# Kernel optimization log

Measured on AMD Instinct MI355X. Metric: run time of the kernel, lower is better.

## Reference

```python
import jax, jax.numpy as jnp
import numpy as np

B, C, H, W = 16, 256, 64, 64
E = 8           # num_experts
TOPK = 2
HID = int(C * 2.0)  # hidden_mult = 2.0 -> 512


def setup_inputs() -> dict:
    key = jax.random.key(0)
    ks = jax.random.split(key, 6)
    x = jax.random.normal(ks[0], (B, C, H, W), dtype=jnp.float32)
    Wr = jax.random.normal(ks[1], (C, E), dtype=jnp.float32) * 0.02
    br = jnp.zeros((E,), dtype=jnp.float32)
    W1 = jax.random.normal(ks[2], (E, C, HID), dtype=jnp.float32) * 0.02
    b1 = jnp.zeros((E, HID), dtype=jnp.float32)
    W2 = jax.random.normal(ks[3], (E, HID, C), dtype=jnp.float32) * 0.02
    b2 = jnp.zeros((E, C), dtype=jnp.float32)
    # nn.Parameter(torch.zeros(1)) in the original; use a small random value so
    scale = jax.random.normal(ks[4], (1,), dtype=jnp.float32) * 0.1
    return {"x": x, "Wr": Wr, "br": br, "W1": W1, "b1": b1,
            "W2": W2, "b2": b2, "scale": scale}


def reference(x, Wr, br, W1, b1, W2, b2, scale):
    b, c, h, w = x.shape
    tokens = jnp.transpose(x, (0, 2, 3, 1)).reshape(b, h * w, c)  # (B, T, C)
    logits = tokens @ Wr + br                                      # (B, T, E)
    topv, topi = jax.lax.top_k(logits, TOPK)                       # (B, T, K)
    wts = jax.nn.softmax(topv, axis=-1)                            # (B, T, K)

    out = jnp.zeros_like(tokens)
    num_experts = Wr.shape[1]
    for e in range(num_experts):
        # combine weight for expert e: sum of routing weights where selected
        we = jnp.sum(jnp.where(topi == e, wts, 0.0), axis=-1)      # (B, T)
        hdn = jax.nn.gelu(tokens @ W1[e] + b1[e], approximate=False)
        y = hdn @ W2[e] + b2[e]                                    # (B, T, C)
        out = out + y * we[..., None]

    out = jnp.transpose(out.reshape(b, h, w, c), (0, 3, 1, 2))     # (B, C, H, W)
    return x + scale[0] * out
```

## Files before the change

### kernel.cpp

```cpp
#include <hip/hip_runtime.h>
#include <hip/hip_bf16.h>
#include <math.h>

#define HW   4096
#define CCH  256
#define NE   8
#define HID  512
#define NTOK 65536
#define PADH 260

typedef short s16x8 __attribute__((ext_vector_type(8)));
typedef float f32x4 __attribute__((ext_vector_type(4)));
typedef unsigned short u16x8 __attribute__((ext_vector_type(8)));

__device__ __forceinline__ float fast_gelu(float v) {
    float v2 = v * v;
    float s  = v * fmaf(0.10294324f, v2, 2.3022079f);
    float e  = exp2f(-s);
    return v * __builtin_amdgcn_rcpf(1.0f + e);
}

__device__ __forceinline__ float bfbits2f(unsigned short h) {
    return __uint_as_float(((unsigned)h) << 16);
}

__global__ __launch_bounds__(256) void k_transpose_both(
    const float* __restrict__ W1, const float* __restrict__ W2,
    __hip_bfloat16* __restrict__ w1t, __hip_bfloat16* __restrict__ w2t,
    int* __restrict__ meta)
{
    __shared__ float t[64][65];
    if (blockIdx.x == 0 && threadIdx.x < 16) meta[threadIdx.x] = 0;
    int bb = blockIdx.x;
    const float* in; __hip_bfloat16* out; int R, CC;
    if (bb < 256) { in = W1; out = w1t; R = 256; CC = 512; }
    else          { in = W2; out = w2t; R = 512; CC = 256; bb -= 256; }
    int tilesC = CC >> 6;
    int per = (R >> 6) * tilesC;
    int e = bb / per, tt = bb % per;
    int r0 = (tt / tilesC) << 6, c0 = (tt % tilesC) << 6;
    const float* ip = in + (size_t)e * R * CC;
    __hip_bfloat16* op = out + (size_t)e * R * CC;
    int lane = threadIdx.x & 63, g = threadIdx.x >> 6;
    for (int i = 0; i < 16; i++) {
        int r = i * 4 + g;
        t[r][lane] = ip[(size_t)(r0 + r) * CC + c0 + lane];
    }
    __syncthreads();
    for (int i = 0; i < 16; i++) {
        int r = i * 4 + g;
        op[(size_t)(c0 + r) * R + r0 + lane] = __float2bfloat16(t[lane][r]);
    }
}

__global__ __launch_bounds__(256) void k_router(
    const float* __restrict__ x, const float* __restrict__ Wr, const float* __restrict__ br,
    __hip_bfloat16* __restrict__ tokens, int* __restrict__ pair, float2* __restrict__ wts,
    int* __restrict__ meta )
{
    __shared__ float xt[CCH][66];
    __shared__ float wr[CCH][NE];
    __shared__ float lg[64][NE];
    __shared__ int lc[NE];
    int tid = threadIdx.x;
    int n0 = blockIdx.x * 64;
    int b = n0 >> 12, p0 = n0 & 4095;
    const float* xb = x + (size_t)b * CCH * HW + p0;
    for (int i = tid; i < CCH * NE; i += 256) ((float*)wr)[i] = Wr[i];
    if (tid < NE) lc[tid] = 0;
    int lane = tid & 63, wv = tid >> 6;
    {
        int j2 = tid & 31, cg = tid >> 5;
        for (int i = 0; i < 32; i++) {
            int c = cg + 8 * i;
            float2 v = *(const float2*)(xb + (size_t)c * HW + 2 * j2);
            *(float2*)&xt[c][2 * j2] = v;
        }
    }
    __syncthreads();
    float a0 = br[2 * wv], a1 = br[2 * wv + 1];
    for (int c = 0; c < CCH; c++) {
        float xv = xt[c][lane];
        a0 = fmaf(xv, wr[c][2 * wv], a0);
        a1 = fmaf(xv, wr[c][2 * wv + 1], a1);
    }
    lg[lane][2 * wv] = a0;
    lg[lane][2 * wv + 1] = a1;
    __syncthreads();
    if (wv == 0) {
        float v0 = -1e30f, v1 = -1e30f; int i0 = 0, i1 = 0;
        for (int e = 0; e < NE; e++) {
            float l = lg[lane][e];
            if (l > v0)      { v1 = v0; i1 = i0; v0 = l; i0 = e; }
            else if (l > v1) { v1 = l; i1 = e; }
        }
        float e1 = expf(v1 - v0);
        float s = 1.0f + e1;
        wts[n0 + lane] = make_float2(1.0f / s, e1 / s);
        pair[n0 + lane] = i0 | (i1 << 8);
        atomicAdd(&lc[i0], 1);
        atomicAdd(&lc[i1], 1);
    }
    __syncthreads();
    if (tid < NE && lc[tid] > 0) atomicAdd(&meta[tid], lc[tid]);
    for (int r = 0; r < 64; r++)
        tokens[(size_t)(n0 + r) * CCH + tid] = __float2bfloat16(xt[tid][r]);
}

__global__ __launch_bounds__(256) void k_scatter(
    const int* __restrict__ pair, const float2* __restrict__ wts,
    int* __restrict__ meta, int* __restrict__ assign_tok, float* __restrict__ assign_w,
    int2* __restrict__ tok_slots)
{
    __shared__ int lcount[NE];
    __shared__ int lbase[NE];
    __shared__ int soff[NE];
    int tid = threadIdx.x;
    int n = blockIdx.x * 256 + tid;
    if (tid < NE) lcount[tid] = 0;
    __syncthreads();
    int pr = pair[n];
    int e0 = pr & 0xff, e1 = (pr >> 8) & 0xff;
    int p0 = atomicAdd(&lcount[e0], 1);
    int p1 = atomicAdd(&lcount[e1], 1);
    __syncthreads();
    if (tid == 0) {
        int off = 0, toff = 0;
        for (int ee = 0; ee < NE; ee++) {
            soff[ee] = off;
            int c = meta[ee];
            if (blockIdx.x == 0) { meta[16 + ee] = off; meta[25 + ee] = toff; }
            off += c;
            toff += (c + 63) >> 6;
        }
        if (blockIdx.x == 0) { meta[24] = off; meta[33] = toff; meta[34] = toff; }
    }
    if (tid < NE) lbase[tid] = atomicAdd(&meta[8 + tid], lcount[tid]);
    __syncthreads();
    float2 w = wts[n];
    int s0 = soff[e0] + lbase[e0] + p0;
    int s1 = soff[e1] + lbase[e1] + p1;
    assign_tok[s0] = n; assign_w[s0] = w.x;
    assign_tok[s1] = n; assign_w[s1] = w.y;
    tok_slots[n] = make_int2(s0, s1);
}

__global__ __launch_bounds__(512, 4) void k_expert(
    const __hip_bfloat16* __restrict__ tokens,
    const __hip_bfloat16* __restrict__ w1t,
    const __hip_bfloat16* __restrict__ w2t,
    const float* __restrict__ b1, const float* __restrict__ b2,
    const int* __restrict__ meta,
    const int* __restrict__ assign_tok, const float* __restrict__ assign_w,
    __hip_bfloat16* __restrict__ ybuf)
{
    __shared__ __align__(16) __hip_bfloat16 Af[64 * 256];
    __shared__ __align__(16) __hip_bfloat16 Hs[64 * PADH];
    __shared__ float wrow[64];
    __shared__ int trow[64];

    int total = meta[34];
    int bid = (blockIdx.x & 7) * 257 + (blockIdx.x >> 3);
    if (bid >= total) return;
    int e = 0;
    while (e < 7 && bid >= meta[25 + e + 1]) e++;
    int tile = bid - meta[25 + e];
    int cnt = meta[e];
    int r0 = tile << 6;
    int abase = meta[16 + e] + r0;
    int nrows = cnt - r0; if (nrows > 64) nrows = 64;

    int tid = threadIdx.x;
    if (tid < 64) {
        if (tid < nrows) { trow[tid] = assign_tok[abase + tid]; wrow[tid] = assign_w[abase + tid]; }
        else             { trow[tid] = 0; wrow[tid] = 0.0f; }
    }
    __syncthreads();

    {
        uint4* dst = (uint4*)Af;
#pragma unroll
        for (int j = 0; j < 4; j++) {
            int row = j * 16 + (tid & 15);
            int chunk = (tid >> 4) & 31;
            dst[j * 512 + tid] = ((const uint4*)(tokens + (size_t)trow[row] * CCH))[chunk];
        }
    }

    int lane = tid & 63, wv = tid >> 6;
    int quad = lane >> 4, l15 = lane & 15;

    const __hip_bfloat16* w1e = w1t + (size_t)e * HID * CCH;
    const __hip_bfloat16* w2e = w2t + (size_t)e * CCH * HID;
    const float* b1e = b1 + e * HID;
    const float* b2e = b2 + e * CCH;

    const s16x8* apb = (const s16x8*)Af + quad * 16 + l15;

    const s16x8* bq0h[2]; const s16x8* bq1h[2];
#pragma unroll
    for (int h = 0; h < 2; h++) {
        int c0 = h * 256 + wv * 32;
        bq0h[h] = (const s16x8*)(w1e + (size_t)(c0)      * CCH + (size_t)l15 * CCH + quad * 8);
        bq1h[h] = (const s16x8*)(w1e + (size_t)(c0 + 16) * CCH + (size_t)l15 * CCH + quad * 8);
    }

    f32x4 oacc[4][2];
#pragma unroll
    for (int i = 0; i < 4; i++)
#pragma unroll
        for (int j = 0; j < 2; j++) oacc[i][j] = (f32x4){0.f, 0.f, 0.f, 0.f};

    s16x8 bf0 = bq0h[0][0], bf1 = bq1h[0][0];
    float ob0 = b2e[wv * 32 + l15];
    float ob1 = b2e[wv * 32 + 16 + l15];

    __syncthreads();

#pragma unroll
    for (int h = 0; h < 2; h++) {
        const s16x8* bq0 = bq0h[h];
        const s16x8* bq1 = bq1h[h];

        f32x4 hacc[4][2];
#pragma unroll
        for (int i = 0; i < 4; i++)
#pragma unroll
            for (int j = 0; j < 2; j++) hacc[i][j] = (f32x4){0.f, 0.f, 0.f, 0.f};

#pragma unroll
        for (int kk = 0; kk < 8; kk++) {
            s16x8 bn0, bn1;
            if (kk < 7) { bn0 = bq0[(kk + 1) * 4]; bn1 = bq1[(kk + 1) * 4]; }
            s16x8 af[4];
#pragma unroll
            for (int mt = 0; mt < 4; mt++) af[mt] = apb[mt * 512 + kk * 4 * 16];
            __builtin_amdgcn_s_setprio(1);
#pragma unroll
            for (int mt = 0; mt < 4; mt++) {
                hacc[mt][0] = __builtin_amdgcn_mfma_f32_16x16x32_bf16(af[mt], bf0, hacc[mt][0], 0, 0, 0);
                hacc[mt][1] = __builtin_amdgcn_mfma_f32_16x16x32_bf16(af[mt], bf1, hacc[mt][1], 0, 0, 0);
            }
            __builtin_amdgcn_s_setprio(0);
            bf0 = bn0; bf1 = bn1;
        }

        const s16x8* b2q0 = (const s16x8*)(w2e + (size_t)(wv * 32      + l15) * HID + h * 256 + quad * 8);
        const s16x8* b2q1 = (const s16x8*)(w2e + (size_t)(wv * 32 + 16 + l15) * HID + h * 256 + quad * 8);
        s16x8 cf0 = b2q0[0], cf1 = b2q1[0];
        float biasA = b1e[h * 256 + wv * 32 + l15];
        float biasB = b1e[h * 256 + wv * 32 + 16 + l15];
        if (h == 0) { bf0 = bq0h[1][0]; bf1 = bq1h[1][0]; }

        if (h == 1) __syncthreads();

#pragma unroll
        for (int nt = 0; nt < 2; nt++) {
            int cl = wv * 32 + nt * 16 + l15;
            float bias = nt ? biasB : biasA;
#pragma unroll
            for (int mt = 0; mt < 4; mt++)
#pragma unroll
                for (int r = 0; r < 4; r++) {
                    int row = mt * 16 + quad * 4 + r;
                    float v = hacc[mt][nt][r] + bias;
                    Hs[row * PADH + cl] = __float2bfloat16(fast_gelu(v));
                }
        }
        __syncthreads();

#pragma unroll
        for (int kk = 0; kk < 8; kk++) {
            s16x8 cn0, cn1;
            if (kk < 7) { cn0 = b2q0[(kk + 1) * 4]; cn1 = b2q1[(kk + 1) * 4]; }
            s16x8 hf[4];
#pragma unroll
            for (int mt = 0; mt < 4; mt++)
                hf[mt] = *(const s16x8*)(Hs + (mt * 16 + l15) * PADH + kk * 32 + quad * 8);
            __builtin_amdgcn_s_setprio(1);
#pragma unroll
            for (int mt = 0; mt < 4; mt++) {
                oacc[mt][0] = __builtin_amdgcn_mfma_f32_16x16x32_bf16(hf[mt], cf0, oacc[mt][0], 0, 0, 0);
                oacc[mt][1] = __builtin_amdgcn_mfma_f32_16x16x32_bf16(hf[mt], cf1, oacc[mt][1], 0, 0, 0);
            }
            __builtin_amdgcn_s_setprio(0);
            cf0 = cn0; cf1 = cn1;
        }
    }

#pragma unroll
    for (int nt = 0; nt < 2; nt++) {
        int cc = wv * 32 + nt * 16 + l15;
        float bias = nt ? ob1 : ob0;
#pragma unroll
        for (int mt = 0; mt < 4; mt++) {
#pragma unroll
            for (int r = 0; r < 4; r++) {
                int row = mt * 16 + quad * 4 + r;
                if (row < nrows) {
                    float v = (oacc[mt][nt][r] + bias) * wrow[row];
                    ybuf[(size_t)(abase + row) * CCH + cc] = __float2bfloat16(v);
                }
            }
        }
    }
}

__global__ __launch_bounds__(256) void k_combine(
    const float* __restrict__ x, const __hip_bfloat16* __restrict__ ybuf,
    const int2* __restrict__ tok_slots, const float* __restrict__ scale,
    float* __restrict__ out)
{
    __shared__ float moe[CCH][33];
    __shared__ int2 slots[32];
    int tid = threadIdx.x;
    int n0 = blockIdx.x * 32;
    if (tid < 32) slots[tid] = tok_slots[n0 + tid];
    __syncthreads();
#pragma unroll
    for (int it = 0; it < 2; it++) {
        int r = (tid >> 4) + 16 * it;
        int g = tid & 15;
        int2 s = slots[r];
        const u16x8* px = (const u16x8*)(ybuf + (size_t)s.x * CCH + 16 * g);
        const u16x8* py = (const u16x8*)(ybuf + (size_t)s.y * CCH + 16 * g);
        u16x8 ax0 = px[0], ax1 = px[1], ay0 = py[0], ay1 = py[1];
#pragma unroll
        for (int k = 0; k < 8; k++) {
            moe[16 * g + k][r]     = bfbits2f(ax0[k]) + bfbits2f(ay0[k]);
            moe[16 * g + 8 + k][r] = bfbits2f(ax1[k]) + bfbits2f(ay1[k]);
        }
    }
    __syncthreads();
    float sc = scale[0];
    int b = n0 >> 12, p0 = n0 & 4095;
    const float* xb = x + (size_t)b * CCH * HW + p0;
    float* ob = out + (size_t)b * CCH * HW + p0;
    int j = tid & 7, cbase = tid >> 3;
#pragma unroll
    for (int i = 0; i < 8; i++) {
        int c = cbase + 32 * i;
        float4 xv = *(const float4*)(xb + (size_t)c * HW + 4 * j);
        float4 o;
        o.x = xv.x + sc * moe[c][4 * j];
        o.y = xv.y + sc * moe[c][4 * j + 1];
        o.z = xv.z + sc * moe[c][4 * j + 2];
        o.w = xv.w + sc * moe[c][4 * j + 3];
        *(float4*)(ob + (size_t)c * HW + 4 * j) = o;
    }
}

extern "C" void kernel_launch(void* const* d_in, const int* in_sizes, int n_in,
                              void* d_out, int out_size, void* d_ws, size_t ws_size,
                              hipStream_t stream)
{
    const float* x     = (const float*)d_in[0];
    const float* Wr    = (const float*)d_in[1];
    const float* br    = (const float*)d_in[2];
    const float* W1    = (const float*)d_in[3];
    const float* b1    = (const float*)d_in[4];
    const float* W2    = (const float*)d_in[5];
    const float* b2    = (const float*)d_in[6];
    const float* scale = (const float*)d_in[7];
    float* out = (float*)d_out;

    char* ws = (char*)d_ws;
    __hip_bfloat16* tokens = (__hip_bfloat16*)(ws);
    __hip_bfloat16* w1t    = (__hip_bfloat16*)(ws + 33554432);
    __hip_bfloat16* w2t    = (__hip_bfloat16*)(ws + 35651584);
    __hip_bfloat16* ybuf   = (__hip_bfloat16*)(ws + 37748736);
    int*    assign_tok = (int*)   (ws + 104857600);
    float*  assign_w   = (float*) (ws + 105381888);
    int2*   tok_slots  = (int2*)  (ws + 105906176);
    int*    pair       = (int*)   (ws + 106430464);
    float2* wts        = (float2*)(ws + 106692608);
    int*    meta       = (int*)   (ws + 107216896);

    k_transpose_both<<<512, 256, 0, stream>>>(W1, W2, w1t, w2t, meta);
    k_router<<<1024, 256, 0, stream>>>(x, Wr, br, tokens, pair, wts, meta);
    k_scatter<<<256, 256, 0, stream>>>(pair, wts, meta, assign_tok, assign_w, tok_slots);
    k_expert<<<2056, 512, 0, stream>>>(tokens, w1t, w2t, b1, b2, meta,
                                       assign_tok, assign_w, ybuf);
    k_combine<<<2048, 256, 0, stream>>>(x, ybuf, tok_slots, scale, out);
}
```

Measured before the change: 339.6 us.

## Vectorize token bf16 stores, alternate expert half order, remap combine LDS writes

The router kernel now writes bf16 tokens as 16-byte vectors per row instead of scalar strided stores. The expert kernel lets blocks alternate which half of the hidden dimension they process first, which spreads weight reads across different address ranges. The combine kernel remaps threads so that consecutive lanes write consecutive token columns in shared memory, to reduce bank conflicts. The vectorized token path reads transposed shared memory by column, which may add LDS bank conflicts.

```diff
diff --git a/kernel.cpp b/kernel.cpp
--- a/kernel.cpp
+++ b/kernel.cpp
@@ -22,6 +22,11 @@
 
 __device__ __forceinline__ float bfbits2f(unsigned short h) {
     return __uint_as_float(((unsigned)h) << 16);
+}
+
+__device__ __forceinline__ short f2bf_bits(float f) {
+    __hip_bfloat16 b = __float2bfloat16(f);
+    return *reinterpret_cast<short*>(&b);
 }
 
 __global__ __launch_bounds__(256) void k_transpose_both(
@@ -103,8 +108,16 @@
     }
     __syncthreads();
     if (tid < NE && lc[tid] > 0) atomicAdd(&meta[tid], lc[tid]);
-    for (int r = 0; r < 64; r++)
-        tokens[(size_t)(n0 + r) * CCH + tid] = __float2bfloat16(xt[tid][r]);
+    {
+        int r = tid & 63, gb = tid >> 6;
+        for (int i = 0; i < 8; i++) {
+            int c0 = gb * 64 + i * 8;
+            s16x8 v;
+#pragma unroll
+            for (int j = 0; j < 8; j++) v[j] = f2bf_bits(xt[c0 + j][r]);
+            *(s16x8*)(tokens + (size_t)(n0 + r) * CCH + c0) = v;
+        }
+    }
 }
 
 __global__ __launch_bounds__(256) void k_scatter(
@@ -160,7 +173,8 @@
     __shared__ int trow[64];
 
     int total = meta[34];
-    int bid = (blockIdx.x & 7) * 257 + (blockIdx.x >> 3);
+    int swz = (int)blockIdx.x;
+    int bid = (swz & 7) * 257 + (swz >> 3);
     if (bid >= total) return;
     int e = 0;
     while (e < 7 && bid >= meta[25 + e + 1]) e++;
@@ -197,13 +211,14 @@
 
     const s16x8* apb = (const s16x8*)Af + quad * 16 + l15;
 
-    const s16x8* bq0h[2]; const s16x8* bq1h[2];
-#pragma unroll
-    for (int h = 0; h < 2; h++) {
-        int c0 = h * 256 + wv * 32;
-        bq0h[h] = (const s16x8*)(w1e + (size_t)(c0)      * CCH + (size_t)l15 * CCH + quad * 8);
-        bq1h[h] = (const s16x8*)(w1e + (size_t)(c0 + 16) * CCH + (size_t)l15 * CCH + quad * 8);
-    }
+    auto G1Q = [&](int h, int off) {
+        return (const s16x8*)(w1e + (size_t)(h * 256 + wv * 32 + off + l15) * CCH) + quad;
+    };
+    auto G2Q = [&](int h, int off) {
+        return (const s16x8*)(w2e + (size_t)(wv * 32 + off + l15) * HID + h * 256) + quad;
+    };
+
+    int hfirst = (swz >> 8) & 1;
 
     f32x4 oacc[4][2];
 #pragma unroll
@@ -211,16 +226,17 @@
 #pragma unroll
         for (int j = 0; j < 2; j++) oacc[i][j] = (f32x4){0.f, 0.f, 0.f, 0.f};
 
-    s16x8 bf0 = bq0h[0][0], bf1 = bq1h[0][0];
+    s16x8 bf0 = G1Q(hfirst, 0)[0], bf1 = G1Q(hfirst, 16)[0];
     float ob0 = b2e[wv * 32 + l15];
     float ob1 = b2e[wv * 32 + 16 + l15];
 
     __syncthreads();
 
 #pragma unroll
-    for (int h = 0; h < 2; h++) {
-        const s16x8* bq0 = bq0h[h];
-        const s16x8* bq1 = bq1h[h];
+    for (int hh = 0; hh < 2; hh++) {
+        int h = hh ^ hfirst;
+        const s16x8* bq0 = G1Q(h, 0);
+        const s16x8* bq1 = G1Q(h, 16);
 
         f32x4 hacc[4][2];
 #pragma unroll
@@ -245,14 +261,14 @@
             bf0 = bn0; bf1 = bn1;
         }
 
-        const s16x8* b2q0 = (const s16x8*)(w2e + (size_t)(wv * 32      + l15) * HID + h * 256 + quad * 8);
-        const s16x8* b2q1 = (const s16x8*)(w2e + (size_t)(wv * 32 + 16 + l15) * HID + h * 256 + quad * 8);
+        const s16x8* b2q0 = G2Q(h, 0);
+        const s16x8* b2q1 = G2Q(h, 16);
         s16x8 cf0 = b2q0[0], cf1 = b2q1[0];
         float biasA = b1e[h * 256 + wv * 32 + l15];
         float biasB = b1e[h * 256 + wv * 32 + 16 + l15];
-        if (h == 0) { bf0 = bq0h[1][0]; bf1 = bq1h[1][0]; }
-
-        if (h == 1) __syncthreads();
+        if (hh == 0) { int h2 = h ^ 1; bf0 = G1Q(h2, 0)[0]; bf1 = G1Q(h2, 16)[0]; }
+
+        if (hh == 1) __syncthreads();
 
 #pragma unroll
         for (int nt = 0; nt < 2; nt++) {
@@ -317,18 +333,20 @@
     int n0 = blockIdx.x * 32;
     if (tid < 32) slots[tid] = tok_slots[n0 + tid];
     __syncthreads();
-#pragma unroll
-    for (int it = 0; it < 2; it++) {
-        int r = (tid >> 4) + 16 * it;
-        int g = tid & 15;
-        int2 s = slots[r];
-        const u16x8* px = (const u16x8*)(ybuf + (size_t)s.x * CCH + 16 * g);
-        const u16x8* py = (const u16x8*)(ybuf + (size_t)s.y * CCH + 16 * g);
-        u16x8 ax0 = px[0], ax1 = px[1], ay0 = py[0], ay1 = py[1];
-#pragma unroll
-        for (int k = 0; k < 8; k++) {
-            moe[16 * g + k][r]     = bfbits2f(ax0[k]) + bfbits2f(ay0[k]);
-            moe[16 * g + 8 + k][r] = bfbits2f(ax1[k]) + bfbits2f(ay1[k]);
+    {
+        int r = tid & 31, g0 = tid >> 5;
+#pragma unroll
+        for (int it = 0; it < 2; it++) {
+            int g = g0 + 8 * it;
+            int2 s = slots[r];
+            const u16x8* px = (const u16x8*)(ybuf + (size_t)s.x * CCH + 16 * g);
+            const u16x8* py = (const u16x8*)(ybuf + (size_t)s.y * CCH + 16 * g);
+            u16x8 ax0 = px[0], ax1 = px[1], ay0 = py[0], ay1 = py[1];
+#pragma unroll
+            for (int k = 0; k < 8; k++) {
+                moe[16 * g + k][r]     = bfbits2f(ax0[k]) + bfbits2f(ay0[k]);
+                moe[16 * g + 8 + k][r] = bfbits2f(ax1[k]) + bfbits2f(ay1[k]);
+            }
         }
     }
     __syncthreads();
```

After: 343.5 us. About the same (+1.2%).
